# Kernel tuning notes

Measured on AMD Instinct MI355X. Metric: run time of the kernel, lower is better.

The kernel has to match this reference:

```python
import jax, jax.numpy as jnp
import numpy as np

B, S, H, NH = 2, 2048, 2048, 16
HD = H // NH
INV_NORM = 1.0 / float(np.sqrt(HD))


def setup_inputs() -> dict:
    key = jax.random.key(0)
    ks = jax.random.split(key, 7)
    hidden_states = jax.random.normal(ks[0], (B, S, H), jnp.float32)
    residual = jax.random.normal(ks[1], (B, S, H), jnp.float32)
    # BLOOM-style alibi bias: [B*NH, 1, S]
    alibi = jax.random.normal(ks[2], (B * NH, 1, S), jnp.float32) * 0.1
    # causal mask: True where attention is NOT allowed
    attention_mask = jnp.triu(jnp.ones((S, S), jnp.bool_), k=1)[None, None]
    attention_mask = jnp.broadcast_to(attention_mask, (B, 1, S, S))
    W_qkv = jax.random.normal(ks[3], (H, 3 * H), jnp.float32) * (1.0 / np.sqrt(H))
    b_qkv = jax.random.normal(ks[4], (3 * H,), jnp.float32) * 0.01
    W_dense = jax.random.normal(ks[5], (H, H), jnp.float32) * (1.0 / np.sqrt(H))
    b_dense = jax.random.normal(ks[6], (H,), jnp.float32) * 0.01
    return {"hidden_states": hidden_states, "residual": residual, "alibi": alibi,
            "attention_mask": attention_mask, "W_qkv": W_qkv, "b_qkv": b_qkv,
            "W_dense": W_dense, "b_dense": b_dense}


def reference(hidden_states, residual, alibi, attention_mask, W_qkv, b_qkv, W_dense, b_dense):
    # fused QKV projection: [B,S,3H] -> [B,S,NH,3,HD]
    qkv = (hidden_states @ W_qkv + b_qkv).reshape(B, S, NH, 3, HD)
    q = qkv[..., 0, :].transpose(0, 2, 1, 3)  # [B,NH,S,HD]
    k = qkv[..., 1, :].transpose(0, 2, 1, 3)
    v = qkv[..., 2, :].transpose(0, 2, 1, 3)
    # baddbmm: alibi + inv_norm * q @ k^T, alibi [B*NH,1,S] broadcasts over query dim
    scores = alibi.reshape(B, NH, 1, S) + INV_NORM * jnp.einsum('bhqd,bhkd->bhqk', q, k)
    scores = jnp.where(attention_mask, jnp.finfo(scores.dtype).min, scores)
    probs = jax.nn.softmax(scores, axis=-1)  # dropout p=0 (eval)
    ctx = jnp.einsum('bhqk,bhkd->bhqd', probs, v)  # [B,NH,S,HD]
    ctx = ctx.transpose(0, 2, 1, 3).reshape(B, S, H)
    out = ctx @ W_dense + b_dense
    return residual + out
```

## Files before the change

kernel.cpp:

```cpp
#include <hip/hip_runtime.h>
#include <stdint.h>

#define SS 2048
#define HH 2048
#define N3H 6144
#define INV_NORM 0.08838834764831845f

typedef __bf16 bf16;
typedef __bf16 bf16x4 __attribute__((ext_vector_type(4)));
typedef __bf16 bf16x8 __attribute__((ext_vector_type(8)));
typedef float  f32x4  __attribute__((ext_vector_type(4)));
typedef uint32_t u32x4 __attribute__((ext_vector_type(4)));

__device__ __forceinline__ void split2(float v, bf16 &hi, bf16 &lo) {
    hi = (bf16)v;
    lo = (bf16)(v - (float)hi);
}

__device__ __forceinline__ void gload16(const void* g, void* l) {
    __builtin_amdgcn_global_load_lds((const __attribute__((address_space(1))) void*)g,
                                     (__attribute__((address_space(3))) void*)l, 16, 0, 0);
}

__global__ __launch_bounds__(256) void k_split_hs(const float* __restrict__ in,
                                                  bf16* __restrict__ oh,
                                                  bf16* __restrict__ ol) {
    int idx = blockIdx.x * 256 + threadIdx.x;
    f32x4 v = ((const f32x4*)in)[idx];
    bf16x4 h, l;
#pragma unroll
    for (int j = 0; j < 4; ++j) { bf16 a, b2; split2(v[j], a, b2); h[j] = a; l[j] = b2; }
    ((bf16x4*)oh)[idx] = h;
    ((bf16x4*)ol)[idx] = l;
}

__global__ __launch_bounds__(256) void k_transpose_split(const float* __restrict__ in,
                                                         bf16* __restrict__ oh,
                                                         bf16* __restrict__ ol,
                                                         int Kin, int Nin) {
    __shared__ float tile[32][33];
    int tx = threadIdx.x & 31, ty = threadIdx.x >> 5;
    int n0 = blockIdx.x * 32, k0 = blockIdx.y * 32;
#pragma unroll
    for (int i = 0; i < 4; ++i) {
        int r = ty + i * 8;
        tile[r][tx] = in[(size_t)(k0 + r) * Nin + n0 + tx];
    }
    __syncthreads();
#pragma unroll
    for (int i = 0; i < 4; ++i) {
        int nl = ty + i * 8;
        float v = tile[tx][nl];
        bf16 h, l; split2(v, h, l);
        size_t o = (size_t)(n0 + nl) * Kin + k0 + tx;
        oh[o] = h; ol[o] = l;
    }
}

template<int MODE>
__global__ __launch_bounds__(256, 3) void k_gemm_bt_x3(
        const bf16* __restrict__ Ah, const bf16* __restrict__ Al,
        const bf16* __restrict__ Bh, const bf16* __restrict__ Bl,
        const float* __restrict__ bias, const float* __restrict__ resid,
        bf16* __restrict__ outH, bf16* __restrict__ outL, float* __restrict__ outF,
        int M, int N, int K) {
    __shared__ __align__(16) uint8_t lds[32768];
    const int tid = threadIdx.x;
    const int nwg = gridDim.x * gridDim.y;
    const int bid = blockIdx.x + gridDim.x * blockIdx.y;
    const int id2 = (bid & 7) * (nwg >> 3) + (bid >> 3);
    const int bx = id2 % gridDim.x, by = id2 / gridDim.x;
    const int m0 = by * 128, n0 = bx * 128;
    const int lane = tid & 63, g = lane >> 4, c = lane & 15, w = tid >> 6;
    const int wm = (w >> 1) * 64, wn = (w & 1) * 64;

    f32x4 acc[4][4] = {};

    const int i0 = tid, i1 = 256 + tid;
    const int r0 = i0 >> 2, p0 = i0 & 3, r1 = i1 >> 2, p1 = i1 & 3;
    const size_t aoff0 = (size_t)(m0 + r0) * K + ((p0 ^ (r0 & 3)) << 3);
    const size_t aoff1 = (size_t)(m0 + r1) * K + ((p1 ^ (r1 & 3)) << 3);
    const size_t boff0 = (size_t)(n0 + r0) * K + ((p0 ^ (r0 & 3)) << 3);
    const size_t boff1 = (size_t)(n0 + r1) * K + ((p1 ^ (r1 & 3)) << 3);
    const uint32_t l0 = (uint32_t)i0 << 4, l1 = (uint32_t)i1 << 4;

    for (int kk = 0; kk < K; kk += 32) {
        __syncthreads();
        gload16(Ah + aoff0 + kk, lds + l0);
        gload16(Ah + aoff1 + kk, lds + l1);
        gload16(Al + aoff0 + kk, lds + 8192 + l0);
        gload16(Al + aoff1 + kk, lds + 8192 + l1);
        gload16(Bh + boff0 + kk, lds + 16384 + l0);
        gload16(Bh + boff1 + kk, lds + 16384 + l1);
        gload16(Bl + boff0 + kk, lds + 24576 + l0);
        gload16(Bl + boff1 + kk, lds + 24576 + l1);
        __syncthreads();

        bf16x8 fah[4], fal[4], fbh[4], fbl[4];
#pragma unroll
        for (int i = 0; i < 4; ++i) {
            int ra = wm + i * 16 + c, rb = wn + i * 16 + c;
            uint32_t oa = (uint32_t)ra * 64 + (uint32_t)((g ^ (ra & 3)) << 4);
            uint32_t ob = (uint32_t)rb * 64 + (uint32_t)((g ^ (rb & 3)) << 4);
            fah[i] = *(const bf16x8*)(lds + oa);
            fal[i] = *(const bf16x8*)(lds + 8192 + oa);
            fbh[i] = *(const bf16x8*)(lds + 16384 + ob);
            fbl[i] = *(const bf16x8*)(lds + 24576 + ob);
        }
#pragma unroll
        for (int i = 0; i < 4; ++i)
#pragma unroll
        for (int j = 0; j < 4; ++j) {
            acc[i][j] = __builtin_amdgcn_mfma_f32_16x16x32_bf16(fah[i], fbh[j], acc[i][j], 0, 0, 0);
            acc[i][j] = __builtin_amdgcn_mfma_f32_16x16x32_bf16(fah[i], fbl[j], acc[i][j], 0, 0, 0);
            acc[i][j] = __builtin_amdgcn_mfma_f32_16x16x32_bf16(fal[i], fbh[j], acc[i][j], 0, 0, 0);
        }
    }

#pragma unroll
    for (int i = 0; i < 4; ++i)
#pragma unroll
    for (int j = 0; j < 4; ++j)
#pragma unroll
    for (int r = 0; r < 4; ++r) {
        int mg = m0 + wm + i * 16 + 4 * g + r;
        int ng = n0 + wn + j * 16 + c;
        float v = acc[i][j][r] + bias[ng];
        size_t o = (size_t)mg * N + ng;
        if (MODE == 0) {
            bf16 h, l; split2(v, h, l);
            outH[o] = h; outL[o] = l;
        } else {
            outF[o] = v + resid[o];
        }
    }
}

__global__ __launch_bounds__(256) void k_attn(const bf16* __restrict__ qkvH,
                                              const bf16* __restrict__ qkvL,
                                              const float* __restrict__ alibi,
                                              bf16* __restrict__ ctxH,
                                              bf16* __restrict__ ctxL) {
    __shared__ __align__(16) uint8_t lds[65536];
    const int tid = threadIdx.x;
    const int bid = blockIdx.x;
    const int bh = bid & 31;
    const int qb = 31 - (bid >> 5);
    const int b = bh >> 4, nh = bh & 15;

    const int w = tid >> 6, lane = tid & 63, g = lane >> 4, cc = lane & 15;
    const int qrow = qb * 64 + w * 16;
    const int nkb = qb + 1;

    bf16x8 qfh[4], qfl[4];
    {
        size_t qo = (size_t)(b * SS + qrow + cc) * N3H + nh * 384;
#pragma unroll
        for (int ks = 0; ks < 4; ++ks) {
            qfh[ks] = *(const bf16x8*)(qkvH + qo + ks * 32 + g * 8);
            qfl[ks] = *(const bf16x8*)(qkvL + qo + ks * 32 + g * 8);
        }
    }

    f32x4 oacc[8] = {};
    float mrow[4] = {-3e38f, -3e38f, -3e38f, -3e38f};
    float lrow[4] = {0.f, 0.f, 0.f, 0.f};
    const float* alrow = alibi + (size_t)bh * SS;
    const uint32_t pbase = (uint32_t)w * 4096;

    const size_t kbase = (size_t)(b * SS) * N3H + nh * 384 + 128;
    int  srow[4]; size_t kof[4]; uint32_t kld[4];
#pragma unroll
    for (int i = 0; i < 4; ++i) {
        int id = i * 256 + tid;
        int r = id >> 4, p = id & 15;
        srow[i] = r;
        kof[i] = (size_t)r * N3H + ((p ^ (r & 7)) << 3);
        kld[i] = (uint32_t)id << 4;
    }

    const int kq = (tid & 15) * 4, d0 = (tid >> 4) * 8;

    for (int kb = 0; kb < nkb; ++kb) {
        __syncthreads();
        {
            size_t base = kbase + (size_t)kb * 64 * N3H;
#pragma unroll
            for (int i = 0; i < 4; ++i) {
                gload16(qkvH + base + kof[i], lds + kld[i]);
                gload16(qkvL + base + kof[i], lds + 16384 + kld[i]);
            }
        }
        {
            bf16x8 vh4[4], vl4[4];
#pragma unroll
            for (int i = 0; i < 4; ++i) {
                size_t go = (size_t)(b * SS + kb * 64 + kq + i) * N3H + nh * 384 + 256 + d0;
                vh4[i] = *(const bf16x8*)(qkvH + go);
                vl4[i] = *(const bf16x8*)(qkvL + go);
            }
#pragma unroll
            for (int j = 0; j < 8; ++j) {
                int d = d0 + j;
                uint32_t off = (uint32_t)d * 128 +
                               (uint32_t)((((kq >> 3) ^ (d & 7)) << 4) + (kq & 7) * 2);
                bf16x4 th = {vh4[0][j], vh4[1][j], vh4[2][j], vh4[3][j]};
                bf16x4 tl = {vl4[0][j], vl4[1][j], vl4[2][j], vl4[3][j]};
                *(bf16x4*)(lds + 32768 + off) = th;
                *(bf16x4*)(lds + 49152 + off) = tl;
            }
        }
        __syncthreads();

        f32x4 sc[4] = {};
        __builtin_amdgcn_s_setprio(1);
#pragma unroll
        for (int nt = 0; nt < 4; ++nt) {
            if (kb * 64 + nt * 16 > qrow + 15) continue;
            int krow = nt * 16 + cc;
#pragma unroll
            for (int ks = 0; ks < 4; ++ks) {
                uint32_t off = (uint32_t)krow * 256 +
                               (uint32_t)(((ks * 4 + g) ^ (krow & 7)) << 4);
                bf16x8 kh  = *(const bf16x8*)(lds + off);
                bf16x8 klv = *(const bf16x8*)(lds + 16384 + off);
                sc[nt] = __builtin_amdgcn_mfma_f32_16x16x32_bf16(qfh[ks], kh,  sc[nt], 0, 0, 0);
                sc[nt] = __builtin_amdgcn_mfma_f32_16x16x32_bf16(qfh[ks], klv, sc[nt], 0, 0, 0);
                sc[nt] = __builtin_amdgcn_mfma_f32_16x16x32_bf16(qfl[ks], kh,  sc[nt], 0, 0, 0);
            }
        }
        __builtin_amdgcn_s_setprio(0);

        float al4[4];
#pragma unroll
        for (int nt = 0; nt < 4; ++nt) al4[nt] = alrow[kb * 64 + nt * 16 + cc];
#pragma unroll
        for (int r = 0; r < 4; ++r) {
            int qg = qrow + 4 * g + r;
            float pm = -3e38f, pv[4];
#pragma unroll
            for (int nt = 0; nt < 4; ++nt) {
                float v = sc[nt][r] * INV_NORM + al4[nt];
                if (kb * 64 + nt * 16 + cc > qg) v = -3e38f;
                pv[nt] = v;
                pm = fmaxf(pm, v);
            }
#pragma unroll
            for (int o2 = 1; o2 < 16; o2 <<= 1) pm = fmaxf(pm, __shfl_xor(pm, o2));
            float mnew = fmaxf(mrow[r], pm);
            float scl = __expf(mrow[r] - mnew);
            mrow[r] = mnew;
            float ps = 0.f;
#pragma unroll
            for (int nt = 0; nt < 4; ++nt) {
                float e = __expf(pv[nt] - mnew);
                sc[nt][r] = e;
                ps += e;
            }
#pragma unroll
            for (int o2 = 1; o2 < 16; o2 <<= 1) ps += __shfl_xor(ps, o2);
            lrow[r] = lrow[r] * scl + ps;
#pragma unroll
            for (int dt = 0; dt < 8; ++dt) oacc[dt][r] *= scl;
        }
        __syncthreads();

#pragma unroll
        for (int r = 0; r < 4; ++r) {
            int prow = 4 * g + r;
#pragma unroll
            for (int nt = 0; nt < 4; ++nt) {
                int col = nt * 16 + cc;
                uint32_t off = (uint32_t)prow * 128 +
                               (uint32_t)((((col >> 3) ^ (prow & 7)) << 4) + (col & 7) * 2);
                bf16 h, l; split2(sc[nt][r], h, l);
                *(bf16*)(lds + pbase + off) = h;
                *(bf16*)(lds + pbase + 2048 + off) = l;
            }
        }
        bf16x8 pah[2], pal[2];
#pragma unroll
        for (int ks = 0; ks < 2; ++ks) {
            uint32_t off = (uint32_t)cc * 128 +
                           (uint32_t)(((ks * 4 + g) ^ (cc & 7)) << 4);
            pah[ks] = *(const bf16x8*)(lds + pbase + off);
            pal[ks] = *(const bf16x8*)(lds + pbase + 2048 + off);
        }
        __builtin_amdgcn_s_setprio(1);
#pragma unroll
        for (int dt = 0; dt < 8; ++dt) {
            int vrow = dt * 16 + cc;
#pragma unroll
            for (int ks = 0; ks < 2; ++ks) {
                uint32_t off = (uint32_t)vrow * 128 +
                               (uint32_t)(((ks * 4 + g) ^ (vrow & 7)) << 4);
                bf16x8 vvh = *(const bf16x8*)(lds + 32768 + off);
                bf16x8 vvl = *(const bf16x8*)(lds + 49152 + off);
                oacc[dt] = __builtin_amdgcn_mfma_f32_16x16x32_bf16(pah[ks], vvh, oacc[dt], 0, 0, 0);
                oacc[dt] = __builtin_amdgcn_mfma_f32_16x16x32_bf16(pah[ks], vvl, oacc[dt], 0, 0, 0);
                oacc[dt] = __builtin_amdgcn_mfma_f32_16x16x32_bf16(pal[ks], vvh, oacc[dt], 0, 0, 0);
            }
        }
        __builtin_amdgcn_s_setprio(0);
    }

#pragma unroll
    for (int r = 0; r < 4; ++r) {
        float inv = 1.0f / lrow[r];
        int qg = qrow + 4 * g + r;
        size_t ob = (size_t)(b * SS + qg) * HH + nh * 128;
#pragma unroll
        for (int dt = 0; dt < 8; ++dt) {
            float v = oacc[dt][r] * inv;
            bf16 h, l; split2(v, h, l);
            ctxH[ob + dt * 16 + cc] = h;
            ctxL[ob + dt * 16 + cc] = l;
        }
    }
}

extern "C" void kernel_launch(void* const* d_in, const int* in_sizes, int n_in,
                              void* d_out, int out_size, void* d_ws, size_t ws_size,
                              hipStream_t stream) {
    const float* hs    = (const float*)d_in[0];
    const float* resid = (const float*)d_in[1];
    const float* alibi = (const float*)d_in[2];
    const float* Wqkv  = (const float*)d_in[4];
    const float* bqkv  = (const float*)d_in[5];
    const float* Wd    = (const float*)d_in[6];
    const float* bd    = (const float*)d_in[7];
    float* out = (float*)d_out;

    char* ws = (char*)d_ws;
    const size_t NEED = 234881024ull;
    if (ws_size < NEED) return;
    bf16* qkvH = (bf16*)(ws);
    bf16* qkvL = (bf16*)(ws + 50331648);
    bf16* Ahh  = (bf16*)(ws + 100663296);
    bf16* All  = (bf16*)(ws + 117440512);
    bf16* WqH  = (bf16*)(ws + 134217728);
    bf16* WqL  = (bf16*)(ws + 159383552);
    bf16* WdH  = (bf16*)(ws + 184549376);
    bf16* WdL  = (bf16*)(ws + 192937984);
    bf16* ctxH = (bf16*)(ws + 201326592);
    bf16* ctxL = (bf16*)(ws + 218103808);

    k_split_hs<<<8192, 256, 0, stream>>>(hs, Ahh, All);
    k_transpose_split<<<dim3(192, 64), 256, 0, stream>>>(Wqkv, WqH, WqL, 2048, 6144);
    k_transpose_split<<<dim3(64, 64), 256, 0, stream>>>(Wd, WdH, WdL, 2048, 2048);
    k_gemm_bt_x3<0><<<dim3(48, 32), 256, 0, stream>>>(Ahh, All, WqH, WqL, bqkv, nullptr,
                                                      qkvH, qkvL, nullptr, 4096, 6144, 2048);
    k_attn<<<1024, 256, 0, stream>>>(qkvH, qkvL, alibi, ctxH, ctxL);
    k_gemm_bt_x3<1><<<dim3(16, 32), 256, 0, stream>>>(ctxH, ctxL, WdH, WdL, bd, resid,
                                                      nullptr, nullptr, out, 4096, 2048, 2048);
}
```

Baseline: 756.7 us.

## Double-buffer LDS in split-bf16 GEMM to overlap global loads with MFMA

The GEMM kernel now uses two 32KB LDS buffers, so the next K-slice is loaded while MFMAs run on the current one, replacing the load-sync-compute-sync loop. It also raises wave priority around the MFMA block with s_setprio. LDS per block doubles and launch bounds drop from 3 to 2 blocks per CU, trading occupancy for latency hiding. An unused srow array in the attention kernel is removed.

```diff
diff --git a/kernel.cpp b/kernel.cpp
--- a/kernel.cpp
+++ b/kernel.cpp
@@ -58,13 +58,13 @@
 }
 
 template<int MODE>
-__global__ __launch_bounds__(256, 3) void k_gemm_bt_x3(
+__global__ __launch_bounds__(256, 2) void k_gemm_bt_x3(
         const bf16* __restrict__ Ah, const bf16* __restrict__ Al,
         const bf16* __restrict__ Bh, const bf16* __restrict__ Bl,
         const float* __restrict__ bias, const float* __restrict__ resid,
         bf16* __restrict__ outH, bf16* __restrict__ outL, float* __restrict__ outF,
         int M, int N, int K) {
-    __shared__ __align__(16) uint8_t lds[32768];
+    __shared__ __align__(16) uint8_t lds[65536];
     const int tid = threadIdx.x;
     const int nwg = gridDim.x * gridDim.y;
     const int bid = blockIdx.x + gridDim.x * blockIdx.y;
@@ -84,29 +84,29 @@
     const size_t boff1 = (size_t)(n0 + r1) * K + ((p1 ^ (r1 & 3)) << 3);
     const uint32_t l0 = (uint32_t)i0 << 4, l1 = (uint32_t)i1 << 4;
 
-    for (int kk = 0; kk < K; kk += 32) {
-        __syncthreads();
-        gload16(Ah + aoff0 + kk, lds + l0);
-        gload16(Ah + aoff1 + kk, lds + l1);
-        gload16(Al + aoff0 + kk, lds + 8192 + l0);
-        gload16(Al + aoff1 + kk, lds + 8192 + l1);
-        gload16(Bh + boff0 + kk, lds + 16384 + l0);
-        gload16(Bh + boff1 + kk, lds + 16384 + l1);
-        gload16(Bl + boff0 + kk, lds + 24576 + l0);
-        gload16(Bl + boff1 + kk, lds + 24576 + l1);
-        __syncthreads();
-
+    auto STAGE = [&](int kk, uint32_t bo) {
+        gload16(Ah + aoff0 + kk, lds + bo + l0);
+        gload16(Ah + aoff1 + kk, lds + bo + l1);
+        gload16(Al + aoff0 + kk, lds + bo + 8192 + l0);
+        gload16(Al + aoff1 + kk, lds + bo + 8192 + l1);
+        gload16(Bh + boff0 + kk, lds + bo + 16384 + l0);
+        gload16(Bh + boff1 + kk, lds + bo + 16384 + l1);
+        gload16(Bl + boff0 + kk, lds + bo + 24576 + l0);
+        gload16(Bl + boff1 + kk, lds + bo + 24576 + l1);
+    };
+    auto COMPUTE = [&](uint32_t bo) {
         bf16x8 fah[4], fal[4], fbh[4], fbl[4];
 #pragma unroll
         for (int i = 0; i < 4; ++i) {
             int ra = wm + i * 16 + c, rb = wn + i * 16 + c;
-            uint32_t oa = (uint32_t)ra * 64 + (uint32_t)((g ^ (ra & 3)) << 4);
-            uint32_t ob = (uint32_t)rb * 64 + (uint32_t)((g ^ (rb & 3)) << 4);
+            uint32_t oa = bo + (uint32_t)ra * 64 + (uint32_t)((g ^ (ra & 3)) << 4);
+            uint32_t ob = bo + (uint32_t)rb * 64 + (uint32_t)((g ^ (rb & 3)) << 4);
             fah[i] = *(const bf16x8*)(lds + oa);
             fal[i] = *(const bf16x8*)(lds + 8192 + oa);
             fbh[i] = *(const bf16x8*)(lds + 16384 + ob);
             fbl[i] = *(const bf16x8*)(lds + 24576 + ob);
         }
+        __builtin_amdgcn_s_setprio(1);
 #pragma unroll
         for (int i = 0; i < 4; ++i)
 #pragma unroll
@@ -115,6 +115,18 @@
             acc[i][j] = __builtin_amdgcn_mfma_f32_16x16x32_bf16(fah[i], fbl[j], acc[i][j], 0, 0, 0);
             acc[i][j] = __builtin_amdgcn_mfma_f32_16x16x32_bf16(fal[i], fbh[j], acc[i][j], 0, 0, 0);
         }
+        __builtin_amdgcn_s_setprio(0);
+    };
+
+    STAGE(0, 0);
+    __syncthreads();
+    for (int kk = 0; kk < K; kk += 64) {
+        STAGE(kk + 32, 32768);
+        COMPUTE(0);
+        __syncthreads();
+        if (kk + 64 < K) STAGE(kk + 64, 0);
+        COMPUTE(32768);
+        __syncthreads();
     }
 
 #pragma unroll
@@ -169,12 +181,11 @@
     const uint32_t pbase = (uint32_t)w * 4096;
 
     const size_t kbase = (size_t)(b * SS) * N3H + nh * 384 + 128;
-    int  srow[4]; size_t kof[4]; uint32_t kld[4];
+    size_t kof[4]; uint32_t kld[4];
 #pragma unroll
     for (int i = 0; i < 4; ++i) {
         int id = i * 256 + tid;
         int r = id >> 4, p = id & 15;
-        srow[i] = r;
         kof[i] = (size_t)r * N3H + ((p ^ (r & 7)) << 3);
         kld[i] = (uint32_t)id << 4;
     }
```

After: 729.5 us. -3.6%, faster.
